# Performance work log

Measured on AMD Instinct MI355X. Metric: run time of the kernel, lower is better.

The kernel has to match this reference:

```python
import jax, jax.numpy as jnp
import numpy as np

VAR = 1.0
STD = float(np.sqrt(VAR))


def setup_inputs() -> dict:
    key = jax.random.key(0)
    k1, k2 = jax.random.split(key)
    n, c = 262144, 100
    scores = jax.random.normal(k1, (n, c), dtype=jnp.float32)
    labels = jax.random.randint(k2, (n,), 0, c, dtype=jnp.int64)
    return {"scores": scores, "labels": labels}


def reference(scores, labels):
    n, c = scores.shape
    # Gaussian pdf over class indices, centered at each label (re_encode_label)
    x = jnp.arange(c, dtype=scores.dtype)[None, :]            # (1, c)
    mu = labels.astype(scores.dtype)[:, None]                  # (n, 1)
    inv_norm = 1.0 / (STD * np.sqrt(2.0 * np.pi))
    code = inv_norm * jnp.exp(-0.5 * ((x - mu) / STD) ** 2)    # (n, c)
    # target distribution: softmax over the (unnormalized) pdf values
    target = jax.nn.softmax(code, axis=1)
    logsfmx = jax.nn.log_softmax(scores, axis=1)
    # KLDivLoss(reduction='batchmean'): sum(target * (log target - input)) / n
    kl = jnp.sum(target * (jnp.log(target) - logsfmx)) / n
    return kl
```

## Files before the change

kernel.cpp:

```cpp
#include <hip/hip_runtime.h>
#include <math.h>

#define C 100
#define WAVES 4
#define ROWS_PER_PASS 64
#define PASSES 4
#define ROWS_PER_BLOCK (ROWS_PER_PASS * PASSES)
#define CHUNKS 25
#define PASS_FLOATS (ROWS_PER_PASS * C)
#define INV_NORM 0.3989422804014327f
#define WFAR     0.67102943f

__device__ __forceinline__ float quad_sum(float x) {
    x += __int_as_float(__builtin_amdgcn_update_dpp(
            0, __float_as_int(x), 0xB1, 0xF, 0xF, true));
    x += __int_as_float(__builtin_amdgcn_update_dpp(
            0, __float_as_int(x), 0x4E, 0xF, 0xF, true));
    return x;
}

__global__ __launch_bounds__(256, 3) void kl_main(
    const float* __restrict__ scores,
    const int*   __restrict__ labels,
    float* __restrict__ out, int n, float inv_n)
{
    __shared__ float buf[2][PASS_FLOATS];
    __shared__ float wpart[WAVES];

    const int tid  = threadIdx.x;
    const int wave = tid >> 6, lane = tid & 63;
    const int r    = lane >> 2, sub  = lane & 3;

    const int blockRow0 = blockIdx.x * ROWS_PER_BLOCK;
    const size_t totalBytes = (size_t)n * C * 4;

    int mu[PASSES];
    #pragma unroll
    for (int p = 0; p < PASSES; ++p) {
        int row = blockRow0 + p * ROWS_PER_PASS + wave * 16 + r;
        mu[p] = (row < n) ? labels[row] : 0;
    }

    float acc = 0.f;

    auto stage = [&](int p, int b) {
        const size_t byteBase = (size_t)(blockRow0 + p * ROWS_PER_PASS) * (C * 4);
        #pragma unroll
        for (int k = 0; k < 7; ++k) {
            int c = wave + k * WAVES;
            if (c < CHUNKS) {
                size_t off = byteBase + (size_t)c * 1024;
                if (off + 1024 > totalBytes) off = totalBytes - 1024;
                const char* src = (const char*)scores + off + lane * 16;
                __builtin_amdgcn_global_load_lds(
                    (const __attribute__((address_space(1))) void*)src,
                    (__attribute__((address_space(3))) void*)&buf[b][c * 256],
                    16, 0, 0);
            }
        }
    };

    auto consume = [&](int p, int b) {
        const float* sp  = &buf[b][(wave * 16 + r) * C];
        const float* spl = sp + sub * 25;
        float se = 0.f, rs = 0.f;
        #pragma unroll
        for (int i = 0; i < 25; ++i) {
            float s = spl[i];
            se += __expf(s);
            rs += s;
        }
        se = quad_sum(se);
        rs = quad_sum(rs);

        const float WP[7] = {0.32897057f, 0.18369895f, 0.03722540f,
            0.00298049f, 8.9804e-5f, 9.9763e-7f, 4.0768e-9f};
        const float WC[7] = {0.39894228f, 0.20681926f, 0.03823936f,
            0.00298711f, 8.9816e-5f, 9.9765e-7f, 4.0768e-9f};
        float dotw = 0.f, csum = 100.f * WFAR, dotc = 0.f;
        const int m = mu[p];
        #pragma unroll
        for (int d = -6; d <= 6; ++d) {
            int idx  = m + d;
            bool ok  = (unsigned)idx < (unsigned)C;
            float s  = sp[min(max(idx, 0), C - 1)];
            int a    = d < 0 ? -d : d;
            float wv = ok ? WP[a] : 0.f;
            dotw  = fmaf(wv, s, dotw);
            csum += wv;
            dotc += ok ? WC[a] : 0.f;
        }

        int myrow = blockRow0 + p * ROWS_PER_PASS + wave * 16 + r;
        if (sub == 0 && myrow < n) {
            float dot = fmaf(WFAR, rs, dotw);
            acc += (dotc - dot) / csum - INV_NORM - __logf(csum) + __logf(se);
        }
    };

    #define VMBAR(N) do { asm volatile("s_waitcnt vmcnt(" #N ")" ::: "memory"); \
                          __builtin_amdgcn_s_barrier();                          \
                          asm volatile("" ::: "memory"); } while (0)
    #define BAR()    do { asm volatile("" ::: "memory");                         \
                          __builtin_amdgcn_s_barrier();                          \
                          asm volatile("" ::: "memory"); } while (0)

    stage(0, 0);
    stage(1, 1);

    VMBAR(6);
    consume(0, 0);
    BAR();
    stage(2, 0);

    VMBAR(6);
    consume(1, 1);
    BAR();
    stage(3, 1);

    VMBAR(6);
    consume(2, 0);

    VMBAR(0);
    consume(3, 1);

    #undef VMBAR
    #undef BAR

    #pragma unroll
    for (int off = 32; off > 0; off >>= 1)
        acc += __shfl_xor(acc, off, 64);
    if (lane == 0) wpart[wave] = acc;
    __syncthreads();
    if (tid == 0)
        atomicAdd(out, (wpart[0] + wpart[1] + wpart[2] + wpart[3]) * inv_n);
}

extern "C" void kernel_launch(void* const* d_in, const int* in_sizes, int n_in,
                              void* d_out, int out_size, void* d_ws, size_t ws_size,
                              hipStream_t stream)
{
    const float* scores = (const float*)d_in[0];
    const int*   labels = (const int*)d_in[1];
    float*       out    = (float*)d_out;

    int n = in_sizes[0] / C;

    hipMemsetAsync(d_out, 0, sizeof(float) * (size_t)out_size, stream);

    int blocks = (n + ROWS_PER_BLOCK - 1) / ROWS_PER_BLOCK;
    kl_main<<<blocks, 256, 0, stream>>>(scores, labels, out, n, 1.0f / (float)n);
}
```

Measured before the change: 158.0 us.

## Halve rows per pass and use eight lanes per row for higher occupancy

Each pass now stages 32 rows instead of 64, which halves LDS use per block and doubles the block count. The launch bound is raised from 3 to 6 blocks per CU so more loads can be in flight. Each row is now split across 8 lanes, each summing 12 or 13 elements, with an extra shuffle in the reduction. The partial chunk at the end of a pass is loaded by half of wave 0, and the vmcnt waits are retuned to match. The cost is more blocks, more atomics and a slightly longer cross-lane reduction.

```diff
diff --git a/kernel.cpp b/kernel.cpp
--- a/kernel.cpp
+++ b/kernel.cpp
@@ -3,11 +3,11 @@
 
 #define C 100
 #define WAVES 4
-#define ROWS_PER_PASS 64
+#define ROWS_PER_PASS 32
 #define PASSES 4
 #define ROWS_PER_BLOCK (ROWS_PER_PASS * PASSES)
-#define CHUNKS 25
 #define PASS_FLOATS (ROWS_PER_PASS * C)
+#define FULL_CHUNKS 12
 #define INV_NORM 0.3989422804014327f
 #define WFAR     0.67102943f
 
@@ -18,8 +18,13 @@
             0, __float_as_int(x), 0x4E, 0xF, 0xF, true));
     return x;
 }
+__device__ __forceinline__ float oct_sum(float x) {
+    x = quad_sum(x);
+    x += __shfl_xor(x, 4);
+    return x;
+}
 
-__global__ __launch_bounds__(256, 3) void kl_main(
+__global__ __launch_bounds__(256, 6) void kl_main(
     const float* __restrict__ scores,
     const int*   __restrict__ labels,
     float* __restrict__ out, int n, float inv_n)
@@ -29,7 +34,9 @@
 
     const int tid  = threadIdx.x;
     const int wave = tid >> 6, lane = tid & 63;
-    const int r    = lane >> 2, sub  = lane & 3;
+    const int rw   = lane >> 3;
+    const int sub8 = lane & 7;
+    const int rowInPassBase = wave * 8 + rw;
 
     const int blockRow0 = blockIdx.x * ROWS_PER_BLOCK;
     const size_t totalBytes = (size_t)n * C * 4;
@@ -37,7 +44,7 @@
     int mu[PASSES];
     #pragma unroll
     for (int p = 0; p < PASSES; ++p) {
-        int row = blockRow0 + p * ROWS_PER_PASS + wave * 16 + r;
+        int row = blockRow0 + p * ROWS_PER_PASS + rowInPassBase;
         mu[p] = (row < n) ? labels[row] : 0;
     }
 
@@ -46,32 +53,47 @@
     auto stage = [&](int p, int b) {
         const size_t byteBase = (size_t)(blockRow0 + p * ROWS_PER_PASS) * (C * 4);
         #pragma unroll
-        for (int k = 0; k < 7; ++k) {
+        for (int k = 0; k < 3; ++k) {
             int c = wave + k * WAVES;
-            if (c < CHUNKS) {
-                size_t off = byteBase + (size_t)c * 1024;
-                if (off + 1024 > totalBytes) off = totalBytes - 1024;
+            size_t off = byteBase + (size_t)c * 1024;
+            if (off + 1024 > totalBytes) off = totalBytes - 1024;
+            const char* src = (const char*)scores + off + lane * 16;
+            __builtin_amdgcn_global_load_lds(
+                (const __attribute__((address_space(1))) void*)src,
+                (__attribute__((address_space(3))) void*)&buf[b][c * 256],
+                16, 0, 0);
+        }
+        if (wave == 0) {
+            size_t off = byteBase + (size_t)FULL_CHUNKS * 1024;
+            if (off + 512 > totalBytes) off = totalBytes - 512;
+            if (lane < 32) {
                 const char* src = (const char*)scores + off + lane * 16;
                 __builtin_amdgcn_global_load_lds(
                     (const __attribute__((address_space(1))) void*)src,
-                    (__attribute__((address_space(3))) void*)&buf[b][c * 256],
+                    (__attribute__((address_space(3))) void*)&buf[b][FULL_CHUNKS * 256],
                     16, 0, 0);
             }
         }
     };
 
     auto consume = [&](int p, int b) {
-        const float* sp  = &buf[b][(wave * 16 + r) * C];
-        const float* spl = sp + sub * 25;
+        const float* sp = &buf[b][rowInPassBase * C];
+        const int off = sub8 * 13 - max(sub8 - 4, 0);
+        const float* spl = sp + off;
         float se = 0.f, rs = 0.f;
         #pragma unroll
-        for (int i = 0; i < 25; ++i) {
+        for (int i = 0; i < 12; ++i) {
             float s = spl[i];
             se += __expf(s);
             rs += s;
         }
-        se = quad_sum(se);
-        rs = quad_sum(rs);
+        if (sub8 < 4) {
+            float s = spl[12];
+            se += __expf(s);
+            rs += s;
+        }
+        se = oct_sum(se);
+        rs = oct_sum(rs);
 
         const float WP[7] = {0.32897057f, 0.18369895f, 0.03722540f,
             0.00298049f, 8.9804e-5f, 9.9763e-7f, 4.0768e-9f};
@@ -91,8 +113,8 @@
             dotc += ok ? WC[a] : 0.f;
         }
 
-        int myrow = blockRow0 + p * ROWS_PER_PASS + wave * 16 + r;
-        if (sub == 0 && myrow < n) {
+        int myrow = blockRow0 + p * ROWS_PER_PASS + rowInPassBase;
+        if (sub8 == 0 && myrow < n) {
             float dot = fmaf(WFAR, rs, dotw);
             acc += (dotc - dot) / csum - INV_NORM - __logf(csum) + __logf(se);
         }
@@ -108,17 +130,17 @@
     stage(0, 0);
     stage(1, 1);
 
-    VMBAR(6);
+    VMBAR(3);
     consume(0, 0);
     BAR();
     stage(2, 0);
 
-    VMBAR(6);
+    VMBAR(3);
     consume(1, 1);
     BAR();
     stage(3, 1);
 
-    VMBAR(6);
+    VMBAR(3);
     consume(2, 0);
 
     VMBAR(0);
```

Measured after the change: 164.6 us. +4.2%, slower.
